# Performance work log

Measured on AMD Instinct MI355X. Metric: run time of the kernel, lower is better.

The kernel has to match this reference:

```python
import jax, jax.numpy as jnp
import numpy as np

NEG_SLOPE = 0.2

def _gat_conv(x, src, dst, W, a_src, a_dst, b, heads, out_ch, concat):
    N = x.shape[0]
    h = (x @ W).reshape(N, heads, out_ch)                      # [N,H,C]
    al_s = jnp.einsum('nhc,hc->nh', h, a_src)                  # [N,H]
    al_d = jnp.einsum('nhc,hc->nh', h, a_dst)
    e = jax.nn.leaky_relu(al_s[src] + al_d[dst], NEG_SLOPE)    # [E,H]
    emax = jax.ops.segment_max(e, dst, num_segments=N)         # [N,H]
    ex = jnp.exp(e - emax[dst])
    denom = jax.ops.segment_sum(ex, dst, num_segments=N)
    alpha = ex / denom[dst]                                    # [E,H]
    msg = h[src] * alpha[:, :, None]                           # [E,H,C]
    out = jax.ops.segment_sum(msg, dst, num_segments=N)        # [N,H,C]
    if concat:
        out = out.reshape(N, heads * out_ch)
    else:
        out = out.mean(axis=1)
    return out + b

def _add_self_loops(edge_index, N):
    loops = jnp.arange(N, dtype=edge_index.dtype)
    src = jnp.concatenate([edge_index[0], loops])
    dst = jnp.concatenate([edge_index[1], loops])
    return src, dst

def setup_inputs() -> dict:
    key = jax.random.key(0)
    ks = jax.random.split(key, 16)
    N, E, Fin, C, H, G, OUT = 50000, 1600000, 128, 32, 8, 256, 64
    s = 0.05
    inp = {
        'x': jax.random.normal(ks[0], (N, Fin), jnp.float32),
        'edge_index': jax.random.randint(ks[1], (2, E), 0, N, jnp.int64),
        'batch': jnp.sort(jax.random.randint(ks[2], (N,), 0, G, jnp.int64)),
        'W0': jax.random.normal(ks[3], (Fin, H * C), jnp.float32) * s,
        'a_src0': jax.random.normal(ks[4], (H, C), jnp.float32) * s,
        'a_dst0': jax.random.normal(ks[5], (H, C), jnp.float32) * s,
        'b0': jnp.zeros((H * C,), jnp.float32),
        'W1': jax.random.normal(ks[6], (H * C, H * C), jnp.float32) * s,
        'a_src1': jax.random.normal(ks[7], (H, C), jnp.float32) * s,
        'a_dst1': jax.random.normal(ks[8], (H, C), jnp.float32) * s,
        'b1': jnp.zeros((H * C,), jnp.float32),
        'W2': jax.random.normal(ks[9], (H * C, C), jnp.float32) * s,
        'a_src2': jax.random.normal(ks[10], (1, C), jnp.float32) * s,
        'a_dst2': jax.random.normal(ks[11], (1, C), jnp.float32) * s,
        'b2': jnp.zeros((C,), jnp.float32),
        'lin_w': jax.random.normal(ks[12], (C, OUT), jnp.float32) * s,
        'lin_b': jnp.zeros((OUT,), jnp.float32),
    }
    return inp

def reference(x, edge_index, batch, W0, a_src0, a_dst0, b0, W1, a_src1, a_dst1, b1,
              W2, a_src2, a_dst2, b2, lin_w, lin_b):
    N = x.shape[0]
    G = 256
    src, dst = _add_self_loops(edge_index, N)
    h = jax.nn.relu(_gat_conv(x, src, dst, W0, a_src0, a_dst0, b0, 8, 32, True))
    h = jax.nn.relu(_gat_conv(h, src, dst, W1, a_src1, a_dst1, b1, 8, 32, True))
    h = _gat_conv(h, src, dst, W2, a_src2, a_dst2, b2, 1, 32, True)  # heads=1 concat -> [N,32]
    # global mean pool over graphs
    sums = jax.ops.segment_sum(h, batch, num_segments=G)
    cnts = jax.ops.segment_sum(jnp.ones((N,), h.dtype), batch, num_segments=G)
    pooled = sums / jnp.maximum(cnts, 1.0)[:, None]
    return pooled @ lin_w + lin_b
```

## Files before the change

kernel.cpp:

```cpp
#include <hip/hip_runtime.h>
#include <hip/hip_bf16.h>


#define LRELU(x) ((x) >= 0.f ? (x) : 0.2f * (x))

typedef unsigned short ushort8 __attribute__((ext_vector_type(8)));
typedef unsigned short ushort4v __attribute__((ext_vector_type(4)));
typedef __attribute__((ext_vector_type(8))) short bf16x8;
typedef __attribute__((ext_vector_type(4))) float f32x4;

__device__ __forceinline__ float bf2f(unsigned short u) {
    return __uint_as_float(((unsigned)u) << 16);
}
__device__ __forceinline__ unsigned short f2bf(float f) {
    __hip_bfloat16 b = __float2bfloat16(f);
    return *reinterpret_cast<unsigned short*>(&b);
}
__device__ __forceinline__ void gl_lds16(const unsigned short* g, unsigned short* l) {
    __builtin_amdgcn_global_load_lds((const __attribute__((address_space(1))) void*)g,
                                     (__attribute__((address_space(3))) void*)l, 16, 0, 0);
}


__global__ void deg_kernel(const int* __restrict__ dst, int* __restrict__ deg,
                           int E, int N) {
    int i = blockIdx.x * blockDim.x + threadIdx.x;
    if (i < E) atomicAdd(&deg[dst[i]], 1);
    else if (i < E + N) atomicAdd(&deg[i - E], 1);
}

__global__ void scan_kernel(const int* __restrict__ deg, int* __restrict__ rowptr,
                            int n) {
    __shared__ int partial[1024];
    const int tid = threadIdx.x;
    const int chunk = (n + 1023) / 1024;
    const int start = min(tid * chunk, n);
    const int end = min(start + chunk, n);
    int s = 0;
    for (int i = start; i < end; i++) s += deg[i];
    partial[tid] = s;
    __syncthreads();
    for (int o = 1; o < 1024; o <<= 1) {
        int v = (tid >= o) ? partial[tid - o] : 0;
        __syncthreads();
        partial[tid] += v;
        __syncthreads();
    }
    int run = (tid == 0) ? 0 : partial[tid - 1];
    for (int i = start; i < end; i++) { rowptr[i] = run; run += deg[i]; }
    if (tid == 0) rowptr[n] = partial[1023];
}

__global__ void scatter_col_binned(const int* __restrict__ src, const int* __restrict__ dst,
                                   int* __restrict__ rowptr, int* __restrict__ col,
                                   int E, int N, int lo, int hi) {
    int i = blockIdx.x * blockDim.x + threadIdx.x;
    if (i < E) {
        int d = dst[i];
        if (d < lo || d >= hi) return;
        int pos = atomicAdd(&rowptr[d], 1);
        col[pos] = src[i];
    } else if (i < E + N) {
        int d = i - E;
        if (d < lo || d >= hi) return;
        int pos = atomicAdd(&rowptr[d], 1);
        col[pos] = d;
    }
}

__global__ void gstart_kernel(const int* __restrict__ batch, int* __restrict__ gstart,
                              int N, int G) {
    int g = blockIdx.x * blockDim.x + threadIdx.x;
    if (g > G) return;
    int lo = 0, hi = N;
    while (lo < hi) { int mid = (lo + hi) >> 1; if (batch[mid] < g) lo = mid + 1; else hi = mid; }
    gstart[g] = lo;
}


__global__ void round_bf16_kernel(const float* __restrict__ X, unsigned short* __restrict__ o,
                                  int n) {
    int i = blockIdx.x * blockDim.x + threadIdx.x;
    if (i >= n) return;
    o[i] = f2bf(X[i]);
}

__global__ void transT_bf16_kernel(const float* __restrict__ W, unsigned short* __restrict__ t,
                                   int K, int N) {
    int i = blockIdx.x * blockDim.x + threadIdx.x;
    if (i >= N * K) return;
    int n = i / K, k = i - n * K;
    t[i] = f2bf(W[(size_t)k * N + n]);
}


template <int BM, int BN, int WM, int WN>
__global__ __launch_bounds__(256)
void gemm_bf16_1t(const unsigned short* __restrict__ A, const unsigned short* __restrict__ Bt,
                  unsigned short* __restrict__ Cc, int M, int N, int K) {
    constexpr int BK = 64;
    constexpr int MT = WM / 16, NT = WN / 16;
    constexpr int NWX = BN / WN;
    __shared__ __attribute__((aligned(16))) unsigned short Ab[BM][BK];
    __shared__ __attribute__((aligned(16))) unsigned short Bb[BN][BK];
    const int tid = threadIdx.x;
    const int lane = tid & 63;
    const int wave = tid >> 6;
    const int wx = wave % NWX, wy = wave / NWX;
    const int by = blockIdx.y * BM;
    const int bx = blockIdx.x * BN;
    const int r16 = lane & 15, kg = lane >> 4;
    const int srow = lane >> 3, sslot = lane & 7;

    f32x4 acc[MT][NT];
#pragma unroll
    for (int i = 0; i < MT; i++)
#pragma unroll
        for (int j = 0; j < NT; j++) acc[i][j] = (f32x4){0.f, 0.f, 0.f, 0.f};

    for (int k0 = 0; k0 < K; k0 += BK) {
        for (int t = wave; t < BM / 8; t += 4) {
            int gm = by + t * 8 + srow;
            if (gm >= M) gm = M - 1;
            gl_lds16(A + (size_t)gm * K + k0 + sslot * 8, &Ab[t * 8][0]);
        }
        for (int t = wave; t < BN / 8; t += 4) {
            int gn = bx + t * 8 + srow;
            gl_lds16(Bt + (size_t)gn * K + k0 + sslot * 8, &Bb[t * 8][0]);
        }
        __syncthreads();
#pragma unroll
        for (int ks = 0; ks < 2; ks++) {
            bf16x8 bh[NT];
#pragma unroll
            for (int j = 0; j < NT; j++)
                bh[j] = *(const bf16x8*)&Bb[wx * WN + j * 16 + r16][ks * 32 + kg * 8];
#pragma unroll
            for (int i = 0; i < MT; i++) {
                bf16x8 ah = *(const bf16x8*)&Ab[wy * WM + i * 16 + r16][ks * 32 + kg * 8];
#pragma unroll
                for (int j = 0; j < NT; j++)
                    acc[i][j] = __builtin_amdgcn_mfma_f32_16x16x32_bf16(ah, bh[j], acc[i][j], 0, 0, 0);
            }
        }
        __syncthreads();
    }
#pragma unroll
    for (int i = 0; i < MT; i++) {
#pragma unroll
        for (int r = 0; r < 4; r++) {
            int gm = by + wy * WM + i * 16 + kg * 4 + r;
            if (gm >= M) continue;
#pragma unroll
            for (int j = 0; j < NT; j++) {
                int gn = bx + wx * WN + j * 16 + r16;
                Cc[(size_t)gm * N + gn] = f2bf(acc[i][j][r]);
            }
        }
    }
}


template <int H, int C>
__global__ void al_bf16(const unsigned short* __restrict__ hfeat, const float* __restrict__ a_src,
                        const float* __restrict__ a_dst, float* __restrict__ als,
                        float* __restrict__ ald, int N) {
    int i = blockIdx.x * blockDim.x + threadIdx.x;
    if (i >= N * H) return;
    int n = i / H, h = i % H;
    const unsigned short* hp = hfeat + (size_t)n * H * C + h * C;
    float s1 = 0.f, s2 = 0.f;
    for (int c0 = 0; c0 < C; c0 += 8) {
        ushort8 v = *(const ushort8*)(hp + c0);
#pragma unroll
        for (int k = 0; k < 8; k++) {
            float f = bf2f(v[k]);
            s1 += f * a_src[h * C + c0 + k];
            s2 += f * a_dst[h * C + c0 + k];
        }
    }
    als[i] = s1;
    ald[i] = s2;
}


__global__ __launch_bounds__(256)
void gat_agg_w8(const unsigned short* __restrict__ hfeat,
                const float* __restrict__ als, const float* __restrict__ ald,
                const int* __restrict__ rowptr,
                const int* __restrict__ col,
                const float* __restrict__ bias,
                unsigned short* __restrict__ outH,
                int N) {
    constexpr int CAP = 128;
    const int wid = threadIdx.x >> 6;
    const int lane = threadIdx.x & 63;
    const int n = blockIdx.x * 4 + wid;
    __shared__ float se_all[4][CAP * 8];
    __shared__ int scol_all[4][CAP];
    if (n >= N) return;
    float* se = se_all[wid];
    int* scol = scol_all[wid];

    const int r0 = (n == 0) ? 0 : rowptr[n - 1];
    const int deg = rowptr[n] - r0;
    const int dcap = min(deg, CAP);

    for (int j = lane; j < dcap; j += 64) scol[j] = col[r0 + j];

    const int slot = lane >> 3, h = lane & 7;
    const float aldh = ald[(size_t)n * 8 + h];
    float psum = 0.f;
    for (int j = 0; j < deg; j += 8) {
        int e = j + slot;
        if (e < deg) {
            int s = (e < dcap) ? scol[e] : col[r0 + e];
            float ev = als[(size_t)s * 8 + h] + aldh;
            ev = LRELU(ev);
            float w = __expf(ev);
            psum += w;
            if (e < CAP) se[e * 8 + h] = w;
        }
    }
#pragma unroll
    for (int m = 8; m < 64; m <<= 1) psum += __shfl_xor(psum, m);
    const int q = lane >> 3;
    const float sinv = 1.0f / __shfl(psum, q);
    const float aldq = ald[(size_t)n * 8 + q];

    const int cb = lane * 4;
    float a0 = 0.f, a1 = 0.f, a2 = 0.f, a3 = 0.f;
    int j = 0;
    for (; j + 3 < dcap; j += 4) {
        int s0 = __builtin_amdgcn_readfirstlane(scol[j]);
        int s1 = __builtin_amdgcn_readfirstlane(scol[j + 1]);
        int s2 = __builtin_amdgcn_readfirstlane(scol[j + 2]);
        int s3 = __builtin_amdgcn_readfirstlane(scol[j + 3]);
        ushort4v v0 = *(const ushort4v*)(hfeat + (size_t)s0 * 256 + cb);
        ushort4v v1 = *(const ushort4v*)(hfeat + (size_t)s1 * 256 + cb);
        ushort4v v2 = *(const ushort4v*)(hfeat + (size_t)s2 * 256 + cb);
        ushort4v v3 = *(const ushort4v*)(hfeat + (size_t)s3 * 256 + cb);
        float w0 = se[j * 8 + q];
        float w1 = se[j * 8 + 8 + q];
        float w2 = se[j * 8 + 16 + q];
        float w3 = se[j * 8 + 24 + q];
        a0 += bf2f(v0[0]) * w0; a1 += bf2f(v0[1]) * w0; a2 += bf2f(v0[2]) * w0; a3 += bf2f(v0[3]) * w0;
        a0 += bf2f(v1[0]) * w1; a1 += bf2f(v1[1]) * w1; a2 += bf2f(v1[2]) * w1; a3 += bf2f(v1[3]) * w1;
        a0 += bf2f(v2[0]) * w2; a1 += bf2f(v2[1]) * w2; a2 += bf2f(v2[2]) * w2; a3 += bf2f(v2[3]) * w2;
        a0 += bf2f(v3[0]) * w3; a1 += bf2f(v3[1]) * w3; a2 += bf2f(v3[2]) * w3; a3 += bf2f(v3[3]) * w3;
    }
    for (; j < dcap; j++) {
        int s0 = __builtin_amdgcn_readfirstlane(scol[j]);
        ushort4v v0 = *(const ushort4v*)(hfeat + (size_t)s0 * 256 + cb);
        float w0 = se[j * 8 + q];
        a0 += bf2f(v0[0]) * w0; a1 += bf2f(v0[1]) * w0; a2 += bf2f(v0[2]) * w0; a3 += bf2f(v0[3]) * w0;
    }
    for (; j < deg; j++) {
        int s0 = col[r0 + j];
        float ev = als[(size_t)s0 * 8 + q] + aldq;
        ev = LRELU(ev);
        float w0 = __expf(ev);
        ushort4v v0 = *(const ushort4v*)(hfeat + (size_t)s0 * 256 + cb);
        a0 += bf2f(v0[0]) * w0; a1 += bf2f(v0[1]) * w0; a2 += bf2f(v0[2]) * w0; a3 += bf2f(v0[3]) * w0;
    }

    float4 b4 = *(const float4*)&bias[cb];
    float o0 = fmaxf(a0 * sinv + b4.x, 0.f);
    float o1 = fmaxf(a1 * sinv + b4.y, 0.f);
    float o2 = fmaxf(a2 * sinv + b4.z, 0.f);
    float o3 = fmaxf(a3 * sinv + b4.w, 0.f);
    const size_t ob = (size_t)n * 256 + cb;
    *(ushort4v*)&outH[ob] = (ushort4v){f2bf(o0), f2bf(o1), f2bf(o2), f2bf(o3)};
}


__global__ __launch_bounds__(256)
void gat_agg_h1w(const unsigned short* __restrict__ hfeat,
                 const float* __restrict__ als, const float* __restrict__ ald,
                 const int* __restrict__ rowptr, const int* __restrict__ col,
                 const float* __restrict__ bias, float* __restrict__ out, int N) {
    constexpr int CAP = 256;
    const int wid = threadIdx.x >> 6;
    const int lane = threadIdx.x & 63;
    const int n = blockIdx.x * 4 + wid;
    __shared__ float sw_all[4][CAP];
    __shared__ int scol_all[4][CAP];
    if (n >= N) return;
    float* sw = sw_all[wid];
    int* scol = scol_all[wid];

    const int r0 = (n == 0) ? 0 : rowptr[n - 1];
    const int deg = rowptr[n] - r0;
    const int dcap = min(deg, CAP);
    const float aldn = ald[n];

    float lsum = 0.f;
    for (int idx = lane; idx < deg; idx += 64) {
        int s = col[r0 + idx];
        float ev = als[s] + aldn;
        ev = LRELU(ev);
        float w = __expf(ev);
        if (idx < CAP) { sw[idx] = w; scol[idx] = s; }
        lsum += w;
    }
#pragma unroll
    for (int m = 1; m < 64; m <<= 1) lsum += __shfl_xor(lsum, m);
    const float sinv = 1.0f / lsum;

    const int slot = lane >> 3, ch = lane & 7;
    float a0 = 0.f, a1 = 0.f, a2 = 0.f, a3 = 0.f;
    for (int j = 0; j < dcap; j += 8) {
        int e = j + slot;
        int ec = min(e, dcap - 1);
        int s = scol[ec];
        float w = (e < dcap) ? sw[ec] : 0.f;
        ushort4v v = *(const ushort4v*)(hfeat + (size_t)s * 32 + ch * 4);
        a0 += bf2f(v[0]) * w; a1 += bf2f(v[1]) * w;
        a2 += bf2f(v[2]) * w; a3 += bf2f(v[3]) * w;
    }
    for (int j = CAP; j < deg; j += 8) {
        int e = j + slot;
        int ec = min(e, deg - 1);
        int s = col[r0 + ec];
        float w = 0.f;
        if (e < deg) {
            float ev = als[s] + aldn;
            ev = LRELU(ev);
            w = __expf(ev);
        }
        ushort4v v = *(const ushort4v*)(hfeat + (size_t)s * 32 + ch * 4);
        a0 += bf2f(v[0]) * w; a1 += bf2f(v[1]) * w;
        a2 += bf2f(v[2]) * w; a3 += bf2f(v[3]) * w;
    }
#pragma unroll
    for (int m = 8; m < 64; m <<= 1) {
        a0 += __shfl_xor(a0, m);
        a1 += __shfl_xor(a1, m);
        a2 += __shfl_xor(a2, m);
        a3 += __shfl_xor(a3, m);
    }
    if (slot == 0) {
        float4 b4 = *(const float4*)&bias[ch * 4];
        float4 o;
        o.x = a0 * sinv + b4.x;
        o.y = a1 * sinv + b4.y;
        o.z = a2 * sinv + b4.z;
        o.w = a3 * sinv + b4.w;
        *(float4*)&out[(size_t)n * 32 + ch * 4] = o;
    }
}


__global__ __launch_bounds__(256)
void pool_final_kernel(const float* __restrict__ h, const int* __restrict__ gstart,
                       const float* __restrict__ lin_w, const float* __restrict__ lin_b,
                       float* __restrict__ out) {
    const int g = blockIdx.x;
    const int tid = threadIdx.x;
    const int n0 = gstart[g], n1 = gstart[g + 1];
    const int r = tid >> 5, c = tid & 31;
    __shared__ float pp[4][32];
    __shared__ float pm[32];
    float acc = 0.f;
    for (int n = n0 + r; n < n1; n += 8) acc += h[(size_t)n * 32 + c];
    acc += __shfl_xor(acc, 32);
    if ((tid & 63) < 32) pp[tid >> 6][c] = acc;
    __syncthreads();
    if (tid < 32) {
        float s = pp[0][tid] + pp[1][tid] + pp[2][tid] + pp[3][tid];
        pm[tid] = s / fmaxf((float)(n1 - n0), 1.f);
    }
    __syncthreads();
    if (tid < 64) {
        float a = lin_b[tid];
#pragma unroll 8
        for (int cc = 0; cc < 32; cc++) a += pm[cc] * lin_w[cc * 64 + tid];
        out[(size_t)g * 64 + tid] = a;
    }
}


extern "C" void kernel_launch(void* const* d_in, const int* in_sizes, int n_in,
                              void* d_out, int out_size, void* d_ws, size_t ws_size,
                              hipStream_t stream) {
    const float* x     = (const float*)d_in[0];
    const int*   ei    = (const int*)d_in[1];
    const int*   batch = (const int*)d_in[2];
    const float* W0    = (const float*)d_in[3];
    const float* a_s0  = (const float*)d_in[4];
    const float* a_d0  = (const float*)d_in[5];
    const float* b0    = (const float*)d_in[6];
    const float* W1    = (const float*)d_in[7];
    const float* a_s1  = (const float*)d_in[8];
    const float* a_d1  = (const float*)d_in[9];
    const float* b1    = (const float*)d_in[10];
    const float* W2    = (const float*)d_in[11];
    const float* a_s2  = (const float*)d_in[12];
    const float* a_d2  = (const float*)d_in[13];
    const float* b2    = (const float*)d_in[14];
    const float* lin_w = (const float*)d_in[15];
    const float* lin_b = (const float*)d_in[16];

    const int N = in_sizes[0] / 128;
    const int E = in_sizes[1] / 2;
    const int G = 256;
    const int Etot = E + N;
    const int* src = ei;
    const int* dst = ei + E;

    char* w = (char*)d_ws;
    size_t off = 0;
    auto alloc = [&](size_t bytes) -> void* {
        void* p = (void*)(w + off);
        off += (bytes + 255) & ~(size_t)255;
        return p;
    };
    int* deg    = (int*)alloc((size_t)N * 4);
    int* rowptr = (int*)alloc((size_t)(N + 1) * 4);
    int* colA   = (int*)alloc((size_t)Etot * 4);
    int* gstart = (int*)alloc((size_t)(G + 1) * 4);
    float* als  = (float*)alloc((size_t)N * 8 * 4);
    float* ald  = (float*)alloc((size_t)N * 8 * 4);
    unsigned short* hb  = (unsigned short*)alloc((size_t)N * 256 * 2);
    unsigned short* g0  = (unsigned short*)alloc((size_t)N * 256 * 2);
    float* out2 = (float*)alloc((size_t)N * 32 * 4);
    unsigned short* w0t = (unsigned short*)alloc((size_t)256 * 128 * 2);
    unsigned short* w1t = (unsigned short*)alloc((size_t)256 * 256 * 2);
    unsigned short* w2t = (unsigned short*)alloc((size_t)32 * 256 * 2);
    unsigned short* xb = g0;

    hipMemsetAsync(deg, 0, (size_t)N * 4, stream);

    deg_kernel<<<(Etot + 255) / 256, 256, 0, stream>>>(dst, deg, E, N);
    scan_kernel<<<1, 1024, 0, stream>>>(deg, rowptr, N);
    for (int p = 0; p < 2; p++) {
        int lo = (int)((size_t)N * p / 2);
        int hi = (int)((size_t)N * (p + 1) / 2);
        scatter_col_binned<<<(Etot + 255) / 256, 256, 0, stream>>>(src, dst, rowptr, colA, E, N, lo, hi);
    }
    gstart_kernel<<<2, 256, 0, stream>>>(batch, gstart, N, G);

    round_bf16_kernel<<<(N * 128 + 255) / 256, 256, 0, stream>>>(x, xb, N * 128);
    transT_bf16_kernel<<<(128 * 256 + 255) / 256, 256, 0, stream>>>(W0, w0t, 128, 256);
    transT_bf16_kernel<<<(256 * 256 + 255) / 256, 256, 0, stream>>>(W1, w1t, 256, 256);
    transT_bf16_kernel<<<(256 * 32 + 255) / 256, 256, 0, stream>>>(W2, w2t, 256, 32);

    const int MB = (N + 127) / 128;

    gemm_bf16_1t<128, 128, 64, 64><<<dim3(2, MB), 256, 0, stream>>>(xb, w0t, hb, N, 256, 128);
    al_bf16<8, 32><<<(N * 8 + 255) / 256, 256, 0, stream>>>(hb, a_s0, a_d0, als, ald, N);
    gat_agg_w8<<<(N + 3) / 4, 256, 0, stream>>>(hb, als, ald, rowptr, colA, b0, g0, N);

    gemm_bf16_1t<128, 128, 64, 64><<<dim3(2, MB), 256, 0, stream>>>(g0, w1t, hb, N, 256, 256);
    al_bf16<8, 32><<<(N * 8 + 255) / 256, 256, 0, stream>>>(hb, a_s1, a_d1, als, ald, N);
    gat_agg_w8<<<(N + 3) / 4, 256, 0, stream>>>(hb, als, ald, rowptr, colA, b1, g0, N);

    gemm_bf16_1t<128, 32, 32, 32><<<dim3(1, MB), 256, 0, stream>>>(g0, w2t, hb, N, 32, 256);
    al_bf16<1, 32><<<(N + 255) / 256, 256, 0, stream>>>(hb, a_s2, a_d2, als, ald, N);
    gat_agg_h1w<<<(N + 3) / 4, 256, 0, stream>>>(hb, als, ald, rowptr, colA, b2, out2, N);

    pool_final_kernel<<<G, 256, 0, stream>>>(out2, gstart, lin_w, lin_b, (float*)d_out);
}
```

Measured before the change: 639.9 us.

## Fuse attention logit computation into GEMM epilogue and merge prep kernels

Computes the per-node, per-head source and destination attention logits directly from the fp32 GEMM accumulators in the epilogue, using a 16-lane shuffle reduction. This removes the separate al_bf16 kernels, which re-read the bf16 feature matrix. It also merges the x and weight bf16 conversion and transpose kernels into one prep kernel, and folds the gstart binary search into the scan kernel to cut launches. Logits now come from unrounded fp32 values rather than bf16-rounded features, which slightly changes numerics, and the epilogue does extra shuffles and global loads of the a vectors.

```diff
diff --git a/kernel.cpp b/kernel.cpp
--- a/kernel.cpp
+++ b/kernel.cpp
@@ -29,10 +29,16 @@
     else if (i < E + N) atomicAdd(&deg[i - E], 1);
 }
 
-__global__ void scan_kernel(const int* __restrict__ deg, int* __restrict__ rowptr,
-                            int n) {
+__global__ void scan_kernel(const int* __restrict__ deg, int* __restrict__ rowptr, int n,
+                            const int* __restrict__ batch, int* __restrict__ gstart,
+                            int N, int G) {
+    const int tid = threadIdx.x;
+    if (tid <= G) {
+        int lo = 0, hi = N;
+        while (lo < hi) { int mid = (lo + hi) >> 1; if (batch[mid] < tid) lo = mid + 1; else hi = mid; }
+        gstart[tid] = lo;
+    }
     __shared__ int partial[1024];
-    const int tid = threadIdx.x;
     const int chunk = (n + 1023) / 1024;
     const int start = min(tid * chunk, n);
     const int end = min(start + chunk, n);
@@ -68,39 +74,46 @@
     }
 }
 
-__global__ void gstart_kernel(const int* __restrict__ batch, int* __restrict__ gstart,
-                              int N, int G) {
-    int g = blockIdx.x * blockDim.x + threadIdx.x;
-    if (g > G) return;
-    int lo = 0, hi = N;
-    while (lo < hi) { int mid = (lo + hi) >> 1; if (batch[mid] < g) lo = mid + 1; else hi = mid; }
-    gstart[g] = lo;
-}
-
-
-__global__ void round_bf16_kernel(const float* __restrict__ X, unsigned short* __restrict__ o,
-                                  int n) {
+
+__global__ void prep_kernel(const float* __restrict__ x, const float* __restrict__ W0,
+                            const float* __restrict__ W1, const float* __restrict__ W2,
+                            unsigned short* __restrict__ xb, unsigned short* __restrict__ w0t,
+                            unsigned short* __restrict__ w1t, unsigned short* __restrict__ w2t,
+                            int N) {
     int i = blockIdx.x * blockDim.x + threadIdx.x;
-    if (i >= n) return;
-    o[i] = f2bf(X[i]);
-}
-
-__global__ void transT_bf16_kernel(const float* __restrict__ W, unsigned short* __restrict__ t,
-                                   int K, int N) {
-    int i = blockIdx.x * blockDim.x + threadIdx.x;
-    if (i >= N * K) return;
-    int n = i / K, k = i - n * K;
-    t[i] = f2bf(W[(size_t)k * N + n]);
-}
-
-
-template <int BM, int BN, int WM, int WN>
+    int nx = N * 128;
+    if (i < nx) { xb[i] = f2bf(x[i]); return; }
+    i -= nx;
+    if (i < 256 * 128) {
+        int n = i / 128, k = i - n * 128;
+        w0t[i] = f2bf(W0[(size_t)k * 256 + n]);
+        return;
+    }
+    i -= 256 * 128;
+    if (i < 256 * 256) {
+        int n = i / 256, k = i - n * 256;
+        w1t[i] = f2bf(W1[(size_t)k * 256 + n]);
+        return;
+    }
+    i -= 256 * 256;
+    if (i < 32 * 256) {
+        int n = i / 256, k = i - n * 256;
+        w2t[i] = f2bf(W2[(size_t)k * 32 + n]);
+    }
+}
+
+
+template <int BM, int BN, int WM, int WN, int H>
 __global__ __launch_bounds__(256)
-void gemm_bf16_1t(const unsigned short* __restrict__ A, const unsigned short* __restrict__ Bt,
-                  unsigned short* __restrict__ Cc, int M, int N, int K) {
+void gemm_bf16_al(const unsigned short* __restrict__ A, const unsigned short* __restrict__ Bt,
+                  unsigned short* __restrict__ Cc,
+                  const float* __restrict__ a_src, const float* __restrict__ a_dst,
+                  float* __restrict__ als, float* __restrict__ ald,
+                  int M, int Nn, int K) {
     constexpr int BK = 64;
     constexpr int MT = WM / 16, NT = WN / 16;
     constexpr int NWX = BN / WN;
+    constexpr int NHL = WN / 32;
     __shared__ __attribute__((aligned(16))) unsigned short Ab[BM][BK];
     __shared__ __attribute__((aligned(16))) unsigned short Bb[BN][BK];
     const int tid = threadIdx.x;
@@ -145,42 +158,42 @@
         }
         __syncthreads();
     }
+
+    const int c0 = bx + wx * WN;
 #pragma unroll
     for (int i = 0; i < MT; i++) {
 #pragma unroll
         for (int r = 0; r < 4; r++) {
             int gm = by + wy * WM + i * 16 + kg * 4 + r;
-            if (gm >= M) continue;
+            bool ok = gm < M;
+            float sa[NHL] = {};
+            float sd[NHL] = {};
 #pragma unroll
             for (int j = 0; j < NT; j++) {
-                int gn = bx + wx * WN + j * 16 + r16;
-                Cc[(size_t)gm * N + gn] = f2bf(acc[i][j][r]);
+                int gn = c0 + j * 16 + r16;
+                float v = acc[i][j][r];
+                if (ok) Cc[(size_t)gm * Nn + gn] = f2bf(v);
+                sa[j >> 1] += v * a_src[gn];
+                sd[j >> 1] += v * a_dst[gn];
             }
-        }
-    }
-}
-
-
-template <int H, int C>
-__global__ void al_bf16(const unsigned short* __restrict__ hfeat, const float* __restrict__ a_src,
-                        const float* __restrict__ a_dst, float* __restrict__ als,
-                        float* __restrict__ ald, int N) {
-    int i = blockIdx.x * blockDim.x + threadIdx.x;
-    if (i >= N * H) return;
-    int n = i / H, h = i % H;
-    const unsigned short* hp = hfeat + (size_t)n * H * C + h * C;
-    float s1 = 0.f, s2 = 0.f;
-    for (int c0 = 0; c0 < C; c0 += 8) {
-        ushort8 v = *(const ushort8*)(hp + c0);
-#pragma unroll
-        for (int k = 0; k < 8; k++) {
-            float f = bf2f(v[k]);
-            s1 += f * a_src[h * C + c0 + k];
-            s2 += f * a_dst[h * C + c0 + k];
-        }
-    }
-    als[i] = s1;
-    ald[i] = s2;
+#pragma unroll
+            for (int m = 1; m < 16; m <<= 1) {
+#pragma unroll
+                for (int t = 0; t < NHL; t++) {
+                    sa[t] += __shfl_xor(sa[t], m);
+                    sd[t] += __shfl_xor(sd[t], m);
+                }
+            }
+            if (ok && r16 == 0) {
+#pragma unroll
+                for (int t = 0; t < NHL; t++) {
+                    int hh = (c0 >> 5) + t;
+                    als[(size_t)gm * H + hh] = sa[t];
+                    ald[(size_t)gm * H + hh] = sd[t];
+                }
+            }
+        }
+    }
 }
 
 
@@ -432,31 +445,30 @@
     hipMemsetAsync(deg, 0, (size_t)N * 4, stream);
 
     deg_kernel<<<(Etot + 255) / 256, 256, 0, stream>>>(dst, deg, E, N);
-    scan_kernel<<<1, 1024, 0, stream>>>(deg, rowptr, N);
+    scan_kernel<<<1, 1024, 0, stream>>>(deg, rowptr, N, batch, gstart, N, G);
     for (int p = 0; p < 2; p++) {
         int lo = (int)((size_t)N * p / 2);
         int hi = (int)((size_t)N * (p + 1) / 2);
         scatter_col_binned<<<(Etot + 255) / 256, 256, 0, stream>>>(src, dst, rowptr, colA, E, N, lo, hi);
     }
-    gstart_kernel<<<2, 256, 0, stream>>>(batch, gstart, N, G);
-
-    round_bf16_kernel<<<(N * 128 + 255) / 256, 256, 0, stream>>>(x, xb, N * 128);
-    transT_bf16_kernel<<<(128 * 256 + 255) / 256, 256, 0, stream>>>(W0, w0t, 128, 256);
-    transT_bf16_kernel<<<(256 * 256 + 255) / 256, 256, 0, stream>>>(W1, w1t, 256, 256);
-    transT_bf16_kernel<<<(256 * 32 + 255) / 256, 256, 0, stream>>>(W2, w2t, 256, 32);
+
+    {
+        long long tot = (long long)N * 128 + 256 * 128 + 256 * 256 + 32 * 256;
+        prep_kernel<<<(int)((tot + 255) / 256), 256, 0, stream>>>(x, W0, W1, W2, xb, w0t, w1t, w2t, N);
+    }
 
     const int MB = (N + 127) / 128;
 
-    gemm_bf16_1t<128, 128, 64, 64><<<dim3(2, MB), 256, 0, stream>>>(xb, w0t, hb, N, 256, 128);
-    al_bf16<8, 32><<<(N * 8 + 255) / 256, 256, 0, stream>>>(hb, a_s0, a_d0, als, ald, N);
+    gemm_bf16_al<128, 128, 64, 64, 8><<<dim3(2, MB), 256, 0, stream>>>(
+        xb, w0t, hb, a_s0, a_d0, als, ald, N, 256, 128);
     gat_agg_w8<<<(N + 3) / 4, 256, 0, stream>>>(hb, als, ald, rowptr, colA, b0, g0, N);
 
-    gemm_bf16_1t<128, 128, 64, 64><<<dim3(2, MB), 256, 0, stream>>>(g0, w1t, hb, N, 256, 256);
-    al_bf16<8, 32><<<(N * 8 + 255) / 256, 256, 0, stream>>>(hb, a_s1, a_d1, als, ald, N);
+    gemm_bf16_al<128, 128, 64, 64, 8><<<dim3(2, MB), 256, 0, stream>>>(
+        g0, w1t, hb, a_s1, a_d1, als, ald, N, 256, 256);
     gat_agg_w8<<<(N + 3) / 4, 256, 0, stream>>>(hb, als, ald, rowptr, colA, b1, g0, N);
 
-    gemm_bf16_1t<128, 32, 32, 32><<<dim3(1, MB), 256, 0, stream>>>(g0, w2t, hb, N, 32, 256);
-    al_bf16<1, 32><<<(N + 255) / 256, 256, 0, stream>>>(hb, a_s2, a_d2, als, ald, N);
+    gemm_bf16_al<128, 32, 32, 32, 1><<<dim3(1, MB), 256, 0, stream>>>(
+        g0, w2t, hb, a_s2, a_d2, als, ald, N, 32, 256);
     gat_agg_h1w<<<(N + 3) / 4, 256, 0, stream>>>(hb, als, ald, rowptr, colA, b2, out2, N);
 
     pool_final_kernel<<<G, 256, 0, stream>>>(out2, gstart, lin_w, lin_b, (float*)d_out);
```

Result: faster. 612.8 us (-4.2%).
